# Kernel optimization log

Measured on AMD Instinct MI355X. Metric: run time of the kernel, lower is better.

Reference implementation:

```python
import jax, jax.numpy as jnp
import numpy as np
import math

ROPE_THETA = 10000.0

def apply_rope(t, pos, theta):
    # t: [b, h, s, d_k] with d_k even; pos: [b, s] int
    d_k = t.shape[-1]
    inv_freq = theta ** (-jnp.arange(0, d_k, 2, dtype=jnp.float32) / d_k)  # [d_k/2]
    angles = pos.astype(jnp.float32)[..., None] * inv_freq  # [b, s, d_k/2]
    cos = jnp.cos(angles)[:, None, :, :]  # [b, 1, s, d_k/2]
    sin = jnp.sin(angles)[:, None, :, :]
    t_even = t[..., 0::2]
    t_odd = t[..., 1::2]
    out_even = cos * t_even - sin * t_odd
    out_odd = sin * t_even + cos * t_odd
    # interleave back: [..., d_k/2, 2] -> [..., d_k]
    return jnp.stack([out_even, out_odd], axis=-1).reshape(t.shape)

def setup_inputs() -> dict:
    key = jax.random.key(0)
    k1, k2, k3, k4, k5 = jax.random.split(key, 5)
    b, s, d_model = 2, 2048, 1024
    std = math.sqrt(2.0 / (2 * d_model))
    return {
        "x": jax.random.normal(k1, (b, s, d_model), dtype=jnp.float32),
        "token_positions": jnp.broadcast_to(jnp.arange(s, dtype=jnp.int32), (b, s)),
        "W_Q": jax.random.normal(k2, (d_model, d_model), dtype=jnp.float32) * std,
        "W_K": jax.random.normal(k3, (d_model, d_model), dtype=jnp.float32) * std,
        "W_V": jax.random.normal(k4, (d_model, d_model), dtype=jnp.float32) * std,
        "W_O": jax.random.normal(k5, (d_model, d_model), dtype=jnp.float32) * std,
    }

def reference(x, token_positions, W_Q, W_K, W_V, W_O):
    b, s, d_model = x.shape
    n_heads = 16
    d_k = d_model // n_heads

    def proj(W):
        # x @ W^T then split heads: [b, s, d_model] -> [b, h, s, d_k]
        y = jnp.einsum('bsd,ed->bse', x, W)
        return y.reshape(b, s, n_heads, d_k).transpose(0, 2, 1, 3)

    Q = apply_rope(proj(W_Q), token_positions, ROPE_THETA)
    K = apply_rope(proj(W_K), token_positions, ROPE_THETA)
    V = proj(W_V)

    scores = jnp.einsum('bhqd,bhkd->bhqk', Q, K) / math.sqrt(d_k)
    causal = jnp.tril(jnp.ones((s, s), dtype=bool))  # True = keep
    scores = jnp.where(causal, scores, -jnp.inf)
    attn = jax.nn.softmax(scores, axis=-1)
    out = jnp.einsum('bhqk,bhkd->bhqd', attn, V)
    out = out.transpose(0, 2, 1, 3).reshape(b, s, d_model)  # merge heads
    return jnp.einsum('bse,de->bsd', out, W_O)
```

## Files before the change

### kernel.cpp

```cpp
#include <hip/hip_runtime.h>
#include <hip/hip_bf16.h>

typedef __attribute__((ext_vector_type(8))) short short8;
typedef __attribute__((ext_vector_type(4))) short short4v;
typedef __attribute__((ext_vector_type(4))) float f32x4;

#define LN10000_DIV32 0.2878231366242558f
#define SCALE_Q_LOG2E 0.18033688011112042f
#define EXP_BIAS 12.0f

__device__ __forceinline__ unsigned short f2bf(float f){
  union { float fv; unsigned u; } a; a.fv = f;
  return (unsigned short)((a.u + 0x7fffu + ((a.u >> 16) & 1u)) >> 16);
}

__global__ __launch_bounds__(256) void convert_all(
    const float* __restrict__ x, const float* __restrict__ wq,
    const float* __restrict__ wk, const float* __restrict__ wv,
    const float* __restrict__ wo, unsigned short* __restrict__ dst,
    float2* __restrict__ tab)
{
  size_t t = (size_t)blockIdx.x * 256 + threadIdx.x;
  if (t < 65536UL){
    const int s = (int)(t >> 5), ip = (int)(t & 31);
    float invf = __expf(-(float)ip * LN10000_DIV32);
    float ang = (float)s * invf;
    tab[t] = make_float2(__cosf(ang), __sinf(ang));
  }
  size_t e = t * 8;
  const float* src; size_t off;
  if (e < 4194304UL)      { src = x;  off = e; }
  else if (e < 5242880UL) { src = wq; off = e - 4194304UL; }
  else if (e < 6291456UL) { src = wk; off = e - 5242880UL; }
  else if (e < 7340032UL) { src = wv; off = e - 6291456UL; }
  else                    { src = wo; off = e - 7340032UL; }
  float4 f0 = *(const float4*)(src + off);
  float4 f1 = *(const float4*)(src + off + 4);
  short8 o;
  o[0] = (short)f2bf(f0.x); o[1] = (short)f2bf(f0.y);
  o[2] = (short)f2bf(f0.z); o[3] = (short)f2bf(f0.w);
  o[4] = (short)f2bf(f1.x); o[5] = (short)f2bf(f1.y);
  o[6] = (short)f2bf(f1.z); o[7] = (short)f2bf(f1.w);
  *(short8*)(dst + e) = o;
}

__global__ __launch_bounds__(512, 2) void gemm_qkv(
    const unsigned short* __restrict__ Xb, const unsigned short* __restrict__ Wb,
    const int* __restrict__ positions, const float2* __restrict__ tab,
    unsigned short* __restrict__ Qb, unsigned short* __restrict__ Kb,
    unsigned short* __restrict__ Vtb)
{
  __shared__ __align__(16) unsigned short As[2*8192];
  __shared__ __align__(16) unsigned short Bs[2*12288];
  f32x4 acc[4][3] = {};
  const int tid = threadIdx.x, lane = tid & 63, w = tid >> 6;
  const int wm = w >> 2, wn = w & 3;
  const int fr = lane & 15, fq = lane >> 4;
  const int id  = blockIdx.x;
  const int xcd = id & 7;
  const int lid = id >> 3;
  const int m0 = (lid & 31) * 128;
  const int n0 = (xcd*2 + (lid >> 5)) * 192;

#define STAGE_ALL(kt, buf) do {                                                     \
    _Pragma("unroll")                                                               \
    for (int i_ = 0; i_ < 2; ++i_){                             \
      const int c_ = i_*512 + tid;                                                  \
      const int row_ = c_ >> 3, cd_ = c_ & 7;                                       \
      const int sc_ = (cd_ ^ (row_ & 7)) << 3;                                      \
      const unsigned short* ga_ = Xb + (size_t)(m0 + row_) * 1024 + (kt)*64 + sc_;  \
      __builtin_amdgcn_global_load_lds((const __attribute__((address_space(1))) void*)ga_, \
          (__attribute__((address_space(3))) void*)(As + (buf)*8192 + c_*8), 16, 0, 0);    \
    }                                                                               \
    _Pragma("unroll")                                                               \
    for (int i_ = 0; i_ < 3; ++i_){                             \
      const int c_ = i_*512 + tid;                                                  \
      const int row_ = c_ >> 3, cd_ = c_ & 7;                                       \
      const int sc_ = (cd_ ^ (row_ & 7)) << 3;                                      \
      const unsigned short* gb_ = Wb + (size_t)(n0 + row_) * 1024 + (kt)*64 + sc_;  \
      __builtin_amdgcn_global_load_lds((const __attribute__((address_space(1))) void*)gb_, \
          (__attribute__((address_space(3))) void*)(Bs + (buf)*12288 + c_*8), 16, 0, 0);   \
    }                                                                               \
  } while(0)

  STAGE_ALL(0, 0);

  const int row_a0 = wm*64 + fr;
  const int row_b0 = wn*48 + fr;

  for (int t = 0; t < 16; ++t){
    const int cur = t & 1;
    if (t + 1 < 16){
      STAGE_ALL(t + 1, cur ^ 1);
      asm volatile("s_waitcnt vmcnt(5)" ::: "memory");
    } else {
      asm volatile("s_waitcnt vmcnt(0)" ::: "memory");
    }
    __builtin_amdgcn_s_barrier();
    asm volatile("" ::: "memory");
    const unsigned short* as = As + cur*8192;
    const unsigned short* bs = Bs + cur*12288;
    short8 af[4], bfv[3];

#define LDA(mf_, kh_) do { \
      const int row_ = row_a0 + (mf_)*16; \
      const int c_ = ((kh_)*4 + fq) ^ (row_ & 7); \
      af[mf_] = *(const short8*)(as + row_*64 + c_*8); } while(0)
#define LDB(nf_, kh_) do { \
      const int row_ = row_b0 + (nf_)*16; \
      const int c_ = ((kh_)*4 + fq) ^ (row_ & 7); \
      bfv[nf_] = *(const short8*)(bs + row_*64 + c_*8); } while(0)

    LDA(0,0); LDA(1,0); LDA(2,0); LDA(3,0);
    LDB(0,0); LDB(1,0); LDB(2,0);
    __builtin_amdgcn_s_setprio(1);
    #pragma unroll
    for (int mf = 0; mf < 4; ++mf)
      #pragma unroll
      for (int nf = 0; nf < 3; ++nf)
        acc[mf][nf] = __builtin_amdgcn_mfma_f32_16x16x32_bf16(af[mf], bfv[nf], acc[mf][nf], 0, 0, 0);
    __builtin_amdgcn_s_setprio(0);

    LDA(0,1); LDA(1,1); LDA(2,1); LDA(3,1);
    LDB(0,1); LDB(1,1); LDB(2,1);
    __builtin_amdgcn_s_setprio(1);
    #pragma unroll
    for (int mf = 0; mf < 4; ++mf)
      #pragma unroll
      for (int nf = 0; nf < 3; ++nf)
        acc[mf][nf] = __builtin_amdgcn_mfma_f32_16x16x32_bf16(af[mf], bfv[nf], acc[mf][nf], 0, 0, 0);
    __builtin_amdgcn_s_setprio(0);
    asm volatile("" ::: "memory");
    __builtin_amdgcn_s_barrier();
  }
#undef STAGE_ALL

  #pragma unroll
  for (int mf = 0; mf < 4; ++mf){
    int pm[4];
    #pragma unroll
    for (int r = 0; r < 4; ++r){
      const int m = m0 + wm*64 + mf*16 + fq*4 + r;
      pm[r] = positions[m] & 2047;
    }
    const int mbase = m0 + wm*64 + mf*16 + fq*4;
    const int b = mbase >> 11;
    const int s0 = mbase & 2047;
    #pragma unroll
    for (int nf = 0; nf < 3; ++nf){
      const int n = n0 + wn*48 + nf*16 + fr;
      const int seg = n >> 10;
      const int h = (n & 1023) >> 6, d = n & 63;
      const size_t bh = (size_t)b * 16 + h;
      if (seg == 2){
        short4v pack;
        #pragma unroll
        for (int r = 0; r < 4; ++r)
          pack[r] = (short)f2bf(acc[mf][nf][r]);
        *(short4v*)&Vtb[(bh*64 + d)*2048 + s0] = pack;
      } else {
        const int ip = d >> 1;
        #pragma unroll
        for (int r = 0; r < 4; ++r){
          float v = acc[mf][nf][r];
          float pv = __shfl_xor(v, 1);
          const float2 cs = tab[(pm[r] << 5) + ip];
          float outv = (d & 1) ? (cs.x * v + cs.y * pv)
                               : (cs.x * v - cs.y * pv);
          if (seg == 0) outv *= SCALE_Q_LOG2E;
          const unsigned short ob = f2bf(outv);
          const int s = s0 + r;
          if (seg == 0) Qb[(bh*2048 + s)*64 + d] = ob;
          else          Kb[(bh*2048 + s)*64 + d] = ob;
        }
      }
    }
  }
}

__global__ __launch_bounds__(256) void attn_kernel(
    const unsigned short* __restrict__ Qb, const unsigned short* __restrict__ Kb,
    const unsigned short* __restrict__ Vtb, unsigned short* __restrict__ Ob)
{
  __shared__ __align__(16) unsigned short Ks[2][4096];
  __shared__ __align__(16) unsigned short Vs[2][4096];
  __shared__ __align__(16) unsigned short Plds[4][16][64];

  const int tid = threadIdx.x, lane = tid & 63, w = tid >> 6;
  const int fr = lane & 15, fq = lane >> 4;

  const int i = blockIdx.x;
  const int bh = (i & 7) | (((i >> 3) & 3) << 3);
  const int tile = 31 - (i >> 5);
  const int b = bh >> 4, h = bh & 15;
  const int q0 = tile * 64 + w * 16;
  const size_t qk_base = (size_t)bh * 2048 * 64;
  const unsigned short* kbase = Kb + qk_base;
  const unsigned short* vbase = Vtb + (size_t)bh * 64 * 2048;

  const unsigned short* qp = Qb + qk_base + (size_t)(q0 + fr) * 64 + fq * 8;
  short8 aq0 = *(const short8*)qp;
  short8 aq1 = *(const short8*)(qp + 32);

  f32x4 accO[4] = {};
  float lrun = 0.f;
  const int qrow = q0 + fr;
  const int nt = tile + 1;
  const int sw3 = (fr & 7) << 2;

#define STAGE_KV(t_, buf_) do {                                                     \
    const int kv0_ = (t_) * 64;                                                     \
    _Pragma("unroll")                                                               \
    for (int ii_ = 0; ii_ < 2; ++ii_){                                              \
      const int chunk_ = ii_ * 256 + tid;                                           \
      const int row_ = chunk_ >> 3, cd_ = chunk_ & 7;                               \
      const int sc_ = (cd_ ^ (row_ & 7)) << 3;                                      \
      const unsigned short* ksrc_ = kbase + (size_t)(kv0_ + row_) * 64 + sc_;       \
      const unsigned short* vsrc_ = vbase + (size_t)row_ * 2048 + kv0_ + sc_;       \
      __builtin_amdgcn_global_load_lds((const __attribute__((address_space(1))) void*)ksrc_, \
          (__attribute__((address_space(3))) void*)(&Ks[buf_][0] + chunk_*8), 16, 0, 0);     \
      __builtin_amdgcn_global_load_lds((const __attribute__((address_space(1))) void*)vsrc_, \
          (__attribute__((address_space(3))) void*)(&Vs[buf_][0] + chunk_*8), 16, 0, 0);     \
    }                                                                               \
  } while(0)

  STAGE_KV(0, 0);
  for (int t = 0; t < nt; ++t){
    const int cur = t & 1;
    const int kv0 = t * 64;
    if (t + 1 < nt){
      STAGE_KV(t + 1, cur ^ 1);
      asm volatile("s_waitcnt vmcnt(4)" ::: "memory");
    } else {
      asm volatile("s_waitcnt vmcnt(0)" ::: "memory");
    }
    __builtin_amdgcn_s_barrier();
    asm volatile("" ::: "memory");
    const unsigned short* ks = &Ks[cur][0];
    const unsigned short* vs = &Vs[cur][0];

    f32x4 sT[4];
    #pragma unroll
    for (int kf = 0; kf < 4; ++kf){
      const int row = kf*16 + fr;
      const int swr = row & 7;
      short8 k0 = *(const short8*)(ks + row*64 + ((fq ^ swr) << 3));
      short8 k1 = *(const short8*)(ks + row*64 + (((4 + fq) ^ swr) << 3));
      f32x4 s = {0.f, 0.f, 0.f, 0.f};
      s = __builtin_amdgcn_mfma_f32_16x16x32_bf16(k0, aq0, s, 0, 0, 0);
      s = __builtin_amdgcn_mfma_f32_16x16x32_bf16(k1, aq1, s, 0, 0, 0);
      sT[kf] = s;
    }
    if (t == nt - 1){
      #pragma unroll
      for (int kf = 0; kf < 4; ++kf)
        #pragma unroll
        for (int r = 0; r < 4; ++r){
          const int kvcol = kv0 + kf*16 + fq*4 + r;
          if (kvcol > qrow) sT[kf][r] = -1e30f;
        }
    }
    float p[4][4];
    float rs = 0.f;
    #pragma unroll
    for (int kf = 0; kf < 4; ++kf)
      #pragma unroll
      for (int r = 0; r < 4; ++r){
        p[kf][r] = __builtin_amdgcn_exp2f(sT[kf][r] - EXP_BIAS);
        rs += p[kf][r];
      }
    rs += __shfl_xor(rs, 16);
    rs += __shfl_xor(rs, 32);
    lrun += rs;
    unsigned* prow = (unsigned*)&Plds[w][fr][0];
    #pragma unroll
    for (int kf = 0; kf < 4; ++kf)
      #pragma unroll
      for (int jj = 0; jj < 2; ++jj){
        unsigned pk;
        asm("v_cvt_pk_bf16_f32 %0, %1, %2" : "=v"(pk) : "v"(p[kf][2*jj]), "v"(p[kf][2*jj+1]));
        prow[(kf*8 + fq*2 + jj) ^ sw3] = pk;
      }
    asm volatile("s_waitcnt lgkmcnt(0)" ::: "memory");
    const unsigned* crow = (const unsigned*)&Plds[w][fr][0];
    short8 ap0 = *(const short8*)&crow[(fq*4) ^ sw3];
    short8 ap1 = *(const short8*)&crow[(16 + fq*4) ^ sw3];
    __builtin_amdgcn_s_setprio(1);
    #pragma unroll
    for (int dblk = 0; dblk < 4; ++dblk){
      const int d = dblk*16 + fr;
      const int swd = d & 7;
      short8 bv0 = *(const short8*)(vs + d*64 + ((fq ^ swd) << 3));
      short8 bv1 = *(const short8*)(vs + d*64 + (((4 + fq) ^ swd) << 3));
      accO[dblk] = __builtin_amdgcn_mfma_f32_16x16x32_bf16(ap0, bv0, accO[dblk], 0, 0, 0);
      accO[dblk] = __builtin_amdgcn_mfma_f32_16x16x32_bf16(ap1, bv1, accO[dblk], 0, 0, 0);
    }
    __builtin_amdgcn_s_setprio(0);
    asm volatile("" ::: "memory");
    __builtin_amdgcn_s_barrier();
  }
#undef STAGE_KV
  float lq[4];
  #pragma unroll
  for (int r = 0; r < 4; ++r)
    lq[r] = __shfl(lrun, fq*4 + r);
  #pragma unroll
  for (int dblk = 0; dblk < 4; ++dblk)
    #pragma unroll
    for (int r = 0; r < 4; ++r){
      const int s = q0 + fq*4 + r;
      const float o = accO[dblk][r] / lq[r];
      Ob[((size_t)b*2048 + s)*1024 + h*64 + dblk*16 + fr] = f2bf(o);
    }
}

__global__ __launch_bounds__(256) void gemm_out(
    const unsigned short* __restrict__ Obf, const unsigned short* __restrict__ Wb,
    float* __restrict__ out)
{
  __shared__ __align__(16) unsigned short As[3*4096];
  __shared__ __align__(16) unsigned short Bs[3*2048];
  f32x4 acc[4][2] = {};
  const int tid = threadIdx.x, lane = tid & 63, w = tid >> 6;
  const int wm = w >> 1, wn = w & 1;
  const int fr = lane & 15, fq = lane >> 4;
  const int id  = blockIdx.x;
  const int xcd = id & 7;
  const int lid = id >> 3;
  const int m0 = (xcd*4 + (lid & 3)) * 128;
  const int n0 = (lid >> 2) * 64;
  const int ph = ((fq ^ ((fr + (fr >> 2)) & 3))) * 8;

#define STAGEO(kt, buf) do {                                                        \
    _Pragma("unroll")                                                               \
    for (int i_ = 0; i_ < 2; ++i_){                                                 \
      const int c_ = i_*256 + tid;                                                  \
      const int row_ = c_ >> 2, cd_ = c_ & 3;                                       \
      const int sc_ = ((cd_ ^ ((row_ + (row_ >> 2)) & 3))) << 3;                    \
      const unsigned short* ga_ = Obf + (size_t)(m0 + row_) * 1024 + (kt)*32 + sc_; \
      __builtin_amdgcn_global_load_lds((const __attribute__((address_space(1))) void*)ga_, \
          (__attribute__((address_space(3))) void*)(As + (buf)*4096 + c_*8), 16, 0, 0);    \
    }                                                                               \
    {                                                                               \
      const int c_ = tid;                                                           \
      const int row_ = c_ >> 2, cd_ = c_ & 3;                                       \
      const int sc_ = ((cd_ ^ ((row_ + (row_ >> 2)) & 3))) << 3;                    \
      const unsigned short* gb_ = Wb + (size_t)(n0 + row_) * 1024 + (kt)*32 + sc_;  \
      __builtin_amdgcn_global_load_lds((const __attribute__((address_space(1))) void*)gb_, \
          (__attribute__((address_space(3))) void*)(Bs + (buf)*2048 + c_*8), 16, 0, 0);    \
    }                                                                               \
  } while(0)

  STAGEO(0, 0);
  STAGEO(1, 1);
  for (int t = 0; t < 32; ++t){
    const int cur = t % 3;
    if (t + 2 < 32) STAGEO(t + 2, (t + 2) % 3);
    if (t < 30)       asm volatile("s_waitcnt vmcnt(6)" ::: "memory");
    else if (t == 30) asm volatile("s_waitcnt vmcnt(3)" ::: "memory");
    else              asm volatile("s_waitcnt vmcnt(0)" ::: "memory");
    __builtin_amdgcn_s_barrier();
    asm volatile("" ::: "memory");
    const unsigned short* as = As + cur*4096;
    const unsigned short* bs = Bs + cur*2048;
    short8 af[4], bfv[2];
    #pragma unroll
    for (int mf = 0; mf < 4; ++mf)
      af[mf] = *(const short8*)(as + (wm*64 + mf*16 + fr) * 32 + ph);
    #pragma unroll
    for (int nf = 0; nf < 2; ++nf)
      bfv[nf] = *(const short8*)(bs + (wn*32 + nf*16 + fr) * 32 + ph);
    #pragma unroll
    for (int mf = 0; mf < 4; ++mf)
      #pragma unroll
      for (int nf = 0; nf < 2; ++nf)
        acc[mf][nf] = __builtin_amdgcn_mfma_f32_16x16x32_bf16(af[mf], bfv[nf], acc[mf][nf], 0, 0, 0);
    asm volatile("" ::: "memory");
    __builtin_amdgcn_s_barrier();
  }
#undef STAGEO

  #pragma unroll
  for (int mf = 0; mf < 4; ++mf)
    #pragma unroll
    for (int nf = 0; nf < 2; ++nf){
      const int n = n0 + wn*32 + nf*16 + fr;
      #pragma unroll
      for (int r = 0; r < 4; ++r){
        const int m = m0 + wm*64 + mf*16 + fq*4 + r;
        out[(size_t)m * 1024 + n] = acc[mf][nf][r];
      }
    }
}

extern "C" void kernel_launch(void* const* d_in, const int* in_sizes, int n_in,
                              void* d_out, int out_size, void* d_ws, size_t ws_size,
                              hipStream_t stream) {
  const float* x  = (const float*)d_in[0];
  const int* pos  = (const int*)d_in[1];
  const float* wq = (const float*)d_in[2];
  const float* wk = (const float*)d_in[3];
  const float* wv = (const float*)d_in[4];
  const float* wo = (const float*)d_in[5];
  float* out = (float*)d_out;

  unsigned short* ws = (unsigned short*)d_ws;
  unsigned short* Xb   = ws;
  unsigned short* Wqkv = ws + 4194304UL;
  unsigned short* Wo   = ws + 7340032UL;
  unsigned short* Qb   = ws + 8388608UL;
  unsigned short* Kb   = ws + 12582912UL;
  unsigned short* Vt   = ws + 16777216UL;
  unsigned short* Ob   = ws + 20971520UL;
  float2* tab          = (float2*)(ws + 25165824UL);

  convert_all<<<4096, 256, 0, stream>>>(x, wq, wk, wv, wo, ws, tab);

  gemm_qkv<<<512, 512, 0, stream>>>(Xb, Wqkv, pos, tab, Qb, Kb, Vt);

  attn_kernel<<<1024, 256, 0, stream>>>(Qb, Kb, Vt, Ob);

  gemm_out<<<512, 256, 0, stream>>>(Ob, Wo, out);
}
```

Baseline: 103.4 us.

## Restructure output GEMM to double-buffered K=64 tiles with XOR swizzle

The output projection GEMM now stages 64-wide K tiles in a double buffer instead of 32-wide tiles in a triple buffer. This halves the number of loop iterations and barriers, and uses an 8-chunk XOR swizzle for LDS bank conflicts. It mirrors the QKV GEMM's two-half MFMA structure with s_setprio and adds a minimum-occupancy launch bound. The cost is less prefetch depth (one stage ahead instead of two) and more LDS per block.

```diff
diff --git a/kernel.cpp b/kernel.cpp
--- a/kernel.cpp
+++ b/kernel.cpp
@@ -132,6 +132,8 @@
     __builtin_amdgcn_s_setprio(0);
     asm volatile("" ::: "memory");
     __builtin_amdgcn_s_barrier();
+#undef LDA
+#undef LDB
   }
 #undef STAGE_ALL
 
@@ -314,12 +316,12 @@
     }
 }
 
-__global__ __launch_bounds__(256) void gemm_out(
+__global__ __launch_bounds__(256, 2) void gemm_out(
     const unsigned short* __restrict__ Obf, const unsigned short* __restrict__ Wb,
     float* __restrict__ out)
 {
-  __shared__ __align__(16) unsigned short As[3*4096];
-  __shared__ __align__(16) unsigned short Bs[3*2048];
+  __shared__ __align__(16) unsigned short As[2*8192];
+  __shared__ __align__(16) unsigned short Bs[2*4096];
   f32x4 acc[4][2] = {};
   const int tid = threadIdx.x, lane = tid & 63, w = tid >> 6;
   const int wm = w >> 1, wn = w & 1;
@@ -329,54 +331,79 @@
   const int lid = id >> 3;
   const int m0 = (xcd*4 + (lid & 3)) * 128;
   const int n0 = (lid >> 2) * 64;
-  const int ph = ((fq ^ ((fr + (fr >> 2)) & 3))) * 8;
 
 #define STAGEO(kt, buf) do {                                                        \
     _Pragma("unroll")                                                               \
-    for (int i_ = 0; i_ < 2; ++i_){                                                 \
+    for (int i_ = 0; i_ < 4; ++i_){                             \
       const int c_ = i_*256 + tid;                                                  \
-      const int row_ = c_ >> 2, cd_ = c_ & 3;                                       \
-      const int sc_ = ((cd_ ^ ((row_ + (row_ >> 2)) & 3))) << 3;                    \
-      const unsigned short* ga_ = Obf + (size_t)(m0 + row_) * 1024 + (kt)*32 + sc_; \
+      const int row_ = c_ >> 3, cd_ = c_ & 7;                                       \
+      const int sc_ = (cd_ ^ (row_ & 7)) << 3;                                      \
+      const unsigned short* ga_ = Obf + (size_t)(m0 + row_) * 1024 + (kt)*64 + sc_; \
       __builtin_amdgcn_global_load_lds((const __attribute__((address_space(1))) void*)ga_, \
-          (__attribute__((address_space(3))) void*)(As + (buf)*4096 + c_*8), 16, 0, 0);    \
+          (__attribute__((address_space(3))) void*)(As + (buf)*8192 + c_*8), 16, 0, 0);    \
     }                                                                               \
-    {                                                                               \
-      const int c_ = tid;                                                           \
-      const int row_ = c_ >> 2, cd_ = c_ & 3;                                       \
-      const int sc_ = ((cd_ ^ ((row_ + (row_ >> 2)) & 3))) << 3;                    \
-      const unsigned short* gb_ = Wb + (size_t)(n0 + row_) * 1024 + (kt)*32 + sc_;  \
+    _Pragma("unroll")                                                               \
+    for (int i_ = 0; i_ < 2; ++i_){                              \
+      const int c_ = i_*256 + tid;                                                  \
+      const int row_ = c_ >> 3, cd_ = c_ & 7;                                       \
+      const int sc_ = (cd_ ^ (row_ & 7)) << 3;                                      \
+      const unsigned short* gb_ = Wb + (size_t)(n0 + row_) * 1024 + (kt)*64 + sc_;  \
       __builtin_amdgcn_global_load_lds((const __attribute__((address_space(1))) void*)gb_, \
-          (__attribute__((address_space(3))) void*)(Bs + (buf)*2048 + c_*8), 16, 0, 0);    \
+          (__attribute__((address_space(3))) void*)(Bs + (buf)*4096 + c_*8), 16, 0, 0);    \
     }                                                                               \
   } while(0)
 
   STAGEO(0, 0);
-  STAGEO(1, 1);
-  for (int t = 0; t < 32; ++t){
-    const int cur = t % 3;
-    if (t + 2 < 32) STAGEO(t + 2, (t + 2) % 3);
-    if (t < 30)       asm volatile("s_waitcnt vmcnt(6)" ::: "memory");
-    else if (t == 30) asm volatile("s_waitcnt vmcnt(3)" ::: "memory");
-    else              asm volatile("s_waitcnt vmcnt(0)" ::: "memory");
-    __builtin_amdgcn_s_barrier();
-    asm volatile("" ::: "memory");
-    const unsigned short* as = As + cur*4096;
-    const unsigned short* bs = Bs + cur*2048;
+
+  const int row_a0 = wm*64 + fr;
+  const int row_b0 = wn*32 + fr;
+
+  for (int t = 0; t < 16; ++t){
+    const int cur = t & 1;
+    if (t + 1 < 16){
+      STAGEO(t + 1, cur ^ 1);
+      asm volatile("s_waitcnt vmcnt(6)" ::: "memory");
+    } else {
+      asm volatile("s_waitcnt vmcnt(0)" ::: "memory");
+    }
+    __builtin_amdgcn_s_barrier();
+    asm volatile("" ::: "memory");
+    const unsigned short* as = As + cur*8192;
+    const unsigned short* bs = Bs + cur*4096;
     short8 af[4], bfv[2];
-    #pragma unroll
-    for (int mf = 0; mf < 4; ++mf)
-      af[mf] = *(const short8*)(as + (wm*64 + mf*16 + fr) * 32 + ph);
-    #pragma unroll
-    for (int nf = 0; nf < 2; ++nf)
-      bfv[nf] = *(const short8*)(bs + (wn*32 + nf*16 + fr) * 32 + ph);
+
+#define LDA(mf_, kh_) do { \
+      const int row_ = row_a0 + (mf_)*16; \
+      const int c_ = ((kh_)*4 + fq) ^ (row_ & 7); \
+      af[mf_] = *(const short8*)(as + row_*64 + c_*8); } while(0)
+#define LDB(nf_, kh_) do { \
+      const int row_ = row_b0 + (nf_)*16; \
+      const int c_ = ((kh_)*4 + fq) ^ (row_ & 7); \
+      bfv[nf_] = *(const short8*)(bs + row_*64 + c_*8); } while(0)
+
+    LDA(0,0); LDA(1,0); LDA(2,0); LDA(3,0);
+    LDB(0,0); LDB(1,0);
+    __builtin_amdgcn_s_setprio(1);
     #pragma unroll
     for (int mf = 0; mf < 4; ++mf)
       #pragma unroll
       for (int nf = 0; nf < 2; ++nf)
         acc[mf][nf] = __builtin_amdgcn_mfma_f32_16x16x32_bf16(af[mf], bfv[nf], acc[mf][nf], 0, 0, 0);
-    asm volatile("" ::: "memory");
-    __builtin_amdgcn_s_barrier();
+    __builtin_amdgcn_s_setprio(0);
+
+    LDA(0,1); LDA(1,1); LDA(2,1); LDA(3,1);
+    LDB(0,1); LDB(1,1);
+    __builtin_amdgcn_s_setprio(1);
+    #pragma unroll
+    for (int mf = 0; mf < 4; ++mf)
+      #pragma unroll
+      for (int nf = 0; nf < 2; ++nf)
+        acc[mf][nf] = __builtin_amdgcn_mfma_f32_16x16x32_bf16(af[mf], bfv[nf], acc[mf][nf], 0, 0, 0);
+    __builtin_amdgcn_s_setprio(0);
+    asm volatile("" ::: "memory");
+    __builtin_amdgcn_s_barrier();
+#undef LDA
+#undef LDB
   }
 #undef STAGEO
 
```

Measured after the change: 100.1 us, median of 3. 3.1% less time.
